# Optimization experiments

Hardware: AMD Instinct MI355X
Metric: run time of the kernel (lower is better)

Reference implementation:

```python
import jax, jax.numpy as jnp
import numpy as np

T, B, N_IN, N_OUT = 100, 32, 1024, 512
LR_LTP, LR_LTD = 1e-4, -1e-4
TAU_PRE, TAU_POST, DT = 20.0, 20.0, 1.0
W_MIN, W_MAX = 0.0, 1.0
SPIKE_PROB = 0.05


def setup_inputs() -> dict:
    key = jax.random.key(0)
    k1, k2, k3 = jax.random.split(key, 3)
    weight = jax.random.uniform(k1, (N_OUT, N_IN), dtype=jnp.float32)
    pre_spikes = (jax.random.uniform(k2, (T, B, N_IN)) < SPIKE_PROB).astype(jnp.float32)
    post_spikes = (jax.random.uniform(k3, (T, B, N_OUT)) < SPIKE_PROB).astype(jnp.float32)
    pre_trace = jnp.zeros((B, N_IN), jnp.float32)
    post_trace = jnp.zeros((B, N_OUT), jnp.float32)
    return {"weight": weight, "pre_spikes": pre_spikes, "post_spikes": post_spikes,
            "pre_trace": pre_trace, "post_trace": post_trace}


def reference(weight, pre_spikes, post_spikes, pre_trace, post_trace):
    # weight: [N_out, N_in]; pre_spikes: [T,B,N_in]; post_spikes: [T,B,N_out]
    decay_pre = jnp.exp(jnp.asarray(-DT / TAU_PRE, weight.dtype))
    decay_post = jnp.exp(jnp.asarray(-DT / TAU_POST, weight.dtype))
    # Soft bounds (w_max=1.0 > 0 -> w_max - w; w_min=0.0 not < 0 -> w)
    soft_ltp = W_MAX - weight
    soft_ltd = weight
    Bf = jnp.asarray(pre_spikes.shape[1], weight.dtype)

    def step(carry, xs):
        pre_tr, post_tr, dw = carry
        pre_s, post_s = xs  # [B,N_in], [B,N_out]
        pre_tr = pre_tr * decay_pre + pre_s
        post_tr = post_tr * decay_post + post_s
        # batch-mean of outer products -> [N_out, N_in]
        ltp_mean = jnp.einsum('bo,bi->oi', post_s, pre_tr) / Bf
        ltd_mean = jnp.einsum('bo,bi->oi', post_tr, pre_s) / Bf
        dw = dw + LR_LTP * soft_ltp * ltp_mean + LR_LTD * soft_ltd * ltd_mean
        return (pre_tr, post_tr, dw), None

    init = (pre_trace, post_trace, jnp.zeros_like(weight))
    (pre_tr, post_tr, delta_w), _ = jax.lax.scan(step, init, (pre_spikes, post_spikes))
    return delta_w, pre_tr, post_tr
```

## Files before the change

### kernel.cpp

```cpp
#include <hip/hip_runtime.h>

typedef unsigned short ushort;
typedef unsigned int uint;
typedef __attribute__((ext_vector_type(8))) short short8;
typedef __attribute__((ext_vector_type(4))) float floatx4;

#define T_STEPS 100
#define BATCH   32
#define NIN     1024
#define NOUT    512

#define SEG     112
#define KPAD    (BATCH * SEG)
#define KROWB   (KPAD * 2)
#define KS      16
#define KCHUNK  (KPAD / KS)
#define BK      32

#define LR_LTP  (1e-4f)
#define LR_LTD  (-1e-4f)
#define INV_B   (1.0f / 32.0f)
#define DECAY   0.951229424500714f
#define D28     0.246596963941607f
#define TCH     28
#define NCHUNK  4

#define OFF_PRE  (NOUT * NIN)
#define OFF_POST (OFF_PRE + BATCH * NIN)

#define U_PRST  0
#define U_PRTT  (U_PRST + NIN * KPAD)
#define U_POST  (U_PRTT + NIN * KPAD)
#define U_POTT  (U_POST + NOUT * KPAD)
#define U_END   (U_POTT + NOUT * KPAD)

static __device__ __forceinline__ ushort f2bf(float f) {
    union { float f; unsigned int u; } v; v.f = f;
    unsigned int r = (v.u + 0x7FFFu + ((v.u >> 16) & 1u)) >> 16;
    return (ushort)r;
}

__global__ __launch_bounds__(256) void stdp_traces_t(
    const float* __restrict__ pre_s,
    const float* __restrict__ post_s,
    const float* __restrict__ pre_tr0,
    const float* __restrict__ post_tr0,
    ushort* __restrict__ pre_s_t, ushort* __restrict__ pre_tr_t,
    ushort* __restrict__ post_s_t, ushort* __restrict__ post_tr_t,
    float* __restrict__ out)
{
    __shared__ float Eend[NCHUNK][64];

    const int chain = threadIdx.x & 63;
    const int c     = threadIdx.x >> 6;
    const int g     = blockIdx.x * 64 + chain;

    const float* src; const float* init;
    ushort *dstS, *dstT;
    int id, nch, shift, outoff;
    if (g < BATCH * NIN) {
        src = pre_s;  init = pre_tr0;  dstS = pre_s_t;  dstT = pre_tr_t;
        id = g;               nch = NIN;  shift = 10; outoff = OFF_PRE;
    } else {
        src = post_s; init = post_tr0; dstS = post_s_t; dstT = post_tr_t;
        id = g - BATCH * NIN; nch = NOUT; shift = 9;  outoff = OFF_POST;
    }

    const int stride = BATCH * nch;
    const int t0 = c * TCH;

    float x[TCH];
    uint  sp[TCH / 2];
    #pragma unroll
    for (int m = 0; m < TCH; m += 2) {
        float v0 = (t0 + m     < T_STEPS) ? src[(size_t)(t0 + m)     * stride + id] : 0.f;
        float v1 = (t0 + m + 1 < T_STEPS) ? src[(size_t)(t0 + m + 1) * stride + id] : 0.f;
        x[m] = v0; x[m + 1] = v1;
        sp[m / 2] = (uint)f2bf(v0) | ((uint)f2bf(v1) << 16);
    }

    float e = 0.f;
    #pragma unroll
    for (int m = 0; m < TCH; ++m) { e = e * DECAY + x[m]; x[m] = e; }
    Eend[c][chain] = e;
    __syncthreads();

    float C = init[id];
    for (int cc = 0; cc < c; ++cc) C = C * D28 + Eend[cc][chain];
    float p = C * DECAY;
    #pragma unroll
    for (int m = 0; m < TCH; ++m) { x[m] += p; p *= DECAY; }

    if (c == NCHUNK - 1) out[outoff + id] = x[15];

    uint tp[TCH / 2];
    #pragma unroll
    for (int m = 0; m < TCH; m += 2)
        tp[m / 2] = (uint)f2bf(x[m]) | ((uint)f2bf(x[m + 1]) << 16);

    const int b  = id >> shift;
    const int ch = id & (nch - 1);
    ushort* ps = dstS + (size_t)ch * KPAD + b * SEG + c * TCH;
    ushort* pt = dstT + (size_t)ch * KPAD + b * SEG + c * TCH;
    #pragma unroll
    for (int j = 0; j < 7; ++j) {
        ((uint2*)ps)[j] = make_uint2(sp[2 * j], sp[2 * j + 1]);
        ((uint2*)pt)[j] = make_uint2(tp[2 * j], tp[2 * j + 1]);
    }
}

__global__ __launch_bounds__(256) void stdp_gemm_dual(
    const ushort* __restrict__ post_s_t, const ushort* __restrict__ pre_tr_t,
    const ushort* __restrict__ post_tr_t, const ushort* __restrict__ pre_s_t,
    const float* __restrict__ wmat, float* __restrict__ Spart)
{
    __shared__ ushort AsP[128 * 32];
    __shared__ ushort AsD[128 * 32];
    __shared__ ushort BsP[128 * 32];
    __shared__ ushort BsD[128 * 32];

    const int i0 = blockIdx.x * 128;
    const int o0 = blockIdx.y * 128;
    const int k0 = blockIdx.z * KCHUNK;

    const int tid  = threadIdx.x;
    const int w    = tid >> 6;
    const int lane = tid & 63;
    const int quad = lane >> 4;
    const int l16  = lane & 15;
    const int wm   = w & 1;
    const int wn   = w >> 1;

    floatx4 accP[4][4], accD[4][4];
    const floatx4 zero4 = {0.f, 0.f, 0.f, 0.f};
    #pragma unroll
    for (int mt = 0; mt < 4; ++mt)
        #pragma unroll
        for (int nt = 0; nt < 4; ++nt) { accP[mt][nt] = zero4; accD[mt][nt] = zero4; }

    for (int kb = k0; kb < k0 + KCHUNK; kb += BK) {
        #pragma unroll
        for (int q = 0; q < 2; ++q) {
            const int c   = w * 128 + q * 64 + lane;
            const int row = c >> 2;
            const int kob = (c & 3) * 16;
            const size_t aoff = (size_t)(o0 + row) * KROWB + kb * 2 + kob;
            const size_t boff = (size_t)(i0 + row) * KROWB + kb * 2 + kob;
            const int ldso = w * 2048 + q * 1024;
            __builtin_amdgcn_global_load_lds(
                (const __attribute__((address_space(1))) void*)((const char*)post_s_t + aoff),
                (__attribute__((address_space(3))) void*)((char*)AsP + ldso), 16, 0, 0);
            __builtin_amdgcn_global_load_lds(
                (const __attribute__((address_space(1))) void*)((const char*)post_tr_t + aoff),
                (__attribute__((address_space(3))) void*)((char*)AsD + ldso), 16, 0, 0);
            __builtin_amdgcn_global_load_lds(
                (const __attribute__((address_space(1))) void*)((const char*)pre_tr_t + boff),
                (__attribute__((address_space(3))) void*)((char*)BsP + ldso), 16, 0, 0);
            __builtin_amdgcn_global_load_lds(
                (const __attribute__((address_space(1))) void*)((const char*)pre_s_t + boff),
                (__attribute__((address_space(3))) void*)((char*)BsD + ldso), 16, 0, 0);
        }
        __syncthreads();

        short8 aP[4], aD[4], bP[4], bD[4];
        #pragma unroll
        for (int mt = 0; mt < 4; ++mt) {
            const int r = (wm * 64 + mt * 16 + l16) * 32 + quad * 8;
            aP[mt] = *(const short8*)&AsP[r];
            aD[mt] = *(const short8*)&AsD[r];
        }
        #pragma unroll
        for (int nt = 0; nt < 4; ++nt) {
            const int r = (wn * 64 + nt * 16 + l16) * 32 + quad * 8;
            bP[nt] = *(const short8*)&BsP[r];
            bD[nt] = *(const short8*)&BsD[r];
        }
        #pragma unroll
        for (int mt = 0; mt < 4; ++mt)
            #pragma unroll
            for (int nt = 0; nt < 4; ++nt) {
                accP[mt][nt] = __builtin_amdgcn_mfma_f32_16x16x32_bf16(
                    aP[mt], bP[nt], accP[mt][nt], 0, 0, 0);
                accD[mt][nt] = __builtin_amdgcn_mfma_f32_16x16x32_bf16(
                    aD[mt], bD[nt], accD[mt][nt], 0, 0, 0);
            }
        __syncthreads();
    }

    float* Sz = Spart + (size_t)blockIdx.z * (NOUT * NIN);
    const float c1 = LR_LTP * INV_B;
    const float c2 = LR_LTD * INV_B;
    #pragma unroll
    for (int mt = 0; mt < 4; ++mt) {
        const int obase = o0 + wm * 64 + mt * 16 + quad * 4;
        #pragma unroll
        for (int nt = 0; nt < 4; ++nt) {
            const int i = i0 + wn * 64 + nt * 16 + l16;
            #pragma unroll
            for (int r = 0; r < 4; ++r) {
                const size_t idx = (size_t)(obase + r) * NIN + i;
                const float wv = wmat[idx];
                Sz[idx] = c1 * (1.0f - wv) * accP[mt][nt][r]
                        + c2 * wv          * accD[mt][nt][r];
            }
        }
    }
}

__global__ __launch_bounds__(256) void stdp_finalize(
    const float* __restrict__ Spart, float* __restrict__ out)
{
    const int j = blockIdx.x * blockDim.x + threadIdx.x;
    float4 s = make_float4(0.f, 0.f, 0.f, 0.f);
    #pragma unroll
    for (int z = 0; z < KS; ++z) {
        const float4 p = ((const float4*)(Spart + (size_t)z * (NOUT * NIN)))[j];
        s.x += p.x; s.y += p.y; s.z += p.z; s.w += p.w;
    }
    ((float4*)out)[j] = s;
}

extern "C" void kernel_launch(void* const* d_in, const int* in_sizes, int n_in,
                              void* d_out, int out_size, void* d_ws, size_t ws_size,
                              hipStream_t stream) {
    const float* weight   = (const float*)d_in[0];
    const float* pre_s    = (const float*)d_in[1];
    const float* post_s   = (const float*)d_in[2];
    const float* pre_tr0  = (const float*)d_in[3];
    const float* post_tr0 = (const float*)d_in[4];
    float* out = (float*)d_out;

    ushort* u = (ushort*)d_ws;
    ushort* pre_s_t   = u + U_PRST;
    ushort* pre_tr_t  = u + U_PRTT;
    ushort* post_s_t  = u + U_POST;
    ushort* post_tr_t = u + U_POTT;
    float*  Spart     = (float*)((char*)d_ws + (size_t)U_END * 2);

    stdp_traces_t<<<dim3(BATCH * (NIN + NOUT) / 64), dim3(256), 0, stream>>>(
        pre_s, post_s, pre_tr0, post_tr0,
        pre_s_t, pre_tr_t, post_s_t, post_tr_t, out);

    stdp_gemm_dual<<<dim3(NIN / 128, NOUT / 128, KS), dim3(256), 0, stream>>>(
        post_s_t, pre_tr_t, post_tr_t, pre_s_t, weight, Spart);

    stdp_finalize<<<dim3((NOUT * NIN / 4) / 256), dim3(256), 0, stream>>>(
        Spart, out);
}
```

Baseline: 119.7 us.

## Stage transposed spike/trace tiles in LDS for coalesced writes and pad strides

The trace kernel now writes its bf16 spike and trace rows into shared memory first, then issues 16-byte coalesced stores to the transposed global buffers instead of scattered 8-byte per-thread stores. The K row stride of the transposed buffers is padded from 3584 to 3648 elements, and the per-split partial-sum slabs are offset by 64 floats, to avoid channel/bank aliasing on power-of-two strides. This adds LDS usage and an extra barrier in the trace kernel. The GEMM loads rely on KROWB, so they now read with the padded stride.

```diff
diff --git a/kernel.cpp b/kernel.cpp
--- a/kernel.cpp
+++ b/kernel.cpp
@@ -12,7 +12,8 @@
 
 #define SEG     112
 #define KPAD    (BATCH * SEG)
-#define KROWB   (KPAD * 2)
+#define KSTRIDE 3648
+#define KROWB   (KSTRIDE * 2)
 #define KS      16
 #define KCHUNK  (KPAD / KS)
 #define BK      32
@@ -24,15 +25,17 @@
 #define D28     0.246596963941607f
 #define TCH     28
 #define NCHUNK  4
+#define LROW    120
 
 #define OFF_PRE  (NOUT * NIN)
 #define OFF_POST (OFF_PRE + BATCH * NIN)
 
 #define U_PRST  0
-#define U_PRTT  (U_PRST + NIN * KPAD)
-#define U_POST  (U_PRTT + NIN * KPAD)
-#define U_POTT  (U_POST + NOUT * KPAD)
-#define U_END   (U_POTT + NOUT * KPAD)
+#define U_PRTT  (U_PRST + NIN * KSTRIDE)
+#define U_POST  (U_PRTT + NIN * KSTRIDE)
+#define U_POTT  (U_POST + NOUT * KSTRIDE)
+#define U_END   (U_POTT + NOUT * KSTRIDE)
+#define SLABF   (NOUT * NIN + 64)
 
 static __device__ __forceinline__ ushort f2bf(float f) {
     union { float f; unsigned int u; } v; v.f = f;
@@ -49,6 +52,8 @@
     ushort* __restrict__ post_s_t, ushort* __restrict__ post_tr_t,
     float* __restrict__ out)
 {
+    __shared__ __align__(16) ushort Ls[64 * LROW];
+    __shared__ __align__(16) ushort Lt[64 * LROW];
     __shared__ float Eend[NCHUNK][64];
 
     const int chain = threadIdx.x & 63;
@@ -56,19 +61,16 @@
     const int g     = blockIdx.x * 64 + chain;
 
     const float* src; const float* init;
-    ushort *dstS, *dstT;
-    int id, nch, shift, outoff;
+    int id, stride, outoff;
     if (g < BATCH * NIN) {
-        src = pre_s;  init = pre_tr0;  dstS = pre_s_t;  dstT = pre_tr_t;
-        id = g;               nch = NIN;  shift = 10; outoff = OFF_PRE;
+        src = pre_s;  init = pre_tr0;
+        id = g;               stride = BATCH * NIN;  outoff = OFF_PRE;
     } else {
-        src = post_s; init = post_tr0; dstS = post_s_t; dstT = post_tr_t;
-        id = g - BATCH * NIN; nch = NOUT; shift = 9;  outoff = OFF_POST;
-    }
-
-    const int stride = BATCH * nch;
+        src = post_s; init = post_tr0;
+        id = g - BATCH * NIN; stride = BATCH * NOUT; outoff = OFF_POST;
+    }
+
     const int t0 = c * TCH;
-
     float x[TCH];
     uint  sp[TCH / 2];
     #pragma unroll
@@ -93,19 +95,39 @@
 
     if (c == NCHUNK - 1) out[outoff + id] = x[15];
 
-    uint tp[TCH / 2];
-    #pragma unroll
-    for (int m = 0; m < TCH; m += 2)
-        tp[m / 2] = (uint)f2bf(x[m]) | ((uint)f2bf(x[m + 1]) << 16);
-
-    const int b  = id >> shift;
-    const int ch = id & (nch - 1);
-    ushort* ps = dstS + (size_t)ch * KPAD + b * SEG + c * TCH;
-    ushort* pt = dstT + (size_t)ch * KPAD + b * SEG + c * TCH;
+    {
+        ushort* ls = Ls + chain * LROW + c * TCH;
+        ushort* lt = Lt + chain * LROW + c * TCH;
+        #pragma unroll
+        for (int j = 0; j < 7; ++j) {
+            const float x0 = x[2 * j * 2];
+            (void)x0;
+            ((uint2*)ls)[j] = make_uint2(sp[2 * j], sp[2 * j + 1]);
+            const uint t_lo = (uint)f2bf(x[4 * j])     | ((uint)f2bf(x[4 * j + 1]) << 16);
+            const uint t_hi = (uint)f2bf(x[4 * j + 2]) | ((uint)f2bf(x[4 * j + 3]) << 16);
+            ((uint2*)lt)[j] = make_uint2(t_lo, t_hi);
+        }
+    }
+    __syncthreads();
+
+    int id0 = blockIdx.x * 64;
+    ushort *dS, *dT; int b0, ch0;
+    if (id0 < BATCH * NIN) {
+        b0 = id0 >> 10; ch0 = id0 & 1023; dS = pre_s_t;  dT = pre_tr_t;
+    } else {
+        const int idq = id0 - BATCH * NIN;
+        b0 = idq >> 9;  ch0 = idq & 511;  dS = post_s_t; dT = post_tr_t;
+    }
     #pragma unroll
     for (int j = 0; j < 7; ++j) {
-        ((uint2*)ps)[j] = make_uint2(sp[2 * j], sp[2 * j + 1]);
-        ((uint2*)pt)[j] = make_uint2(tp[2 * j], tp[2 * j + 1]);
+        const int q  = threadIdx.x + 256 * j;
+        const int op = q >= 896;
+        const int qq = q - op * 896;
+        const int r  = qq / 14;
+        const int cc = qq - r * 14;
+        const ushort* lsrc = (op ? Lt : Ls) + r * LROW + cc * 8;
+        ushort* gdst = (op ? dT : dS) + (size_t)(ch0 + r) * KSTRIDE + b0 * SEG + cc * 8;
+        *(uint4*)gdst = *(const uint4*)lsrc;
     }
 }
 
@@ -187,7 +209,7 @@
         __syncthreads();
     }
 
-    float* Sz = Spart + (size_t)blockIdx.z * (NOUT * NIN);
+    float* Sz = Spart + (size_t)blockIdx.z * SLABF;
     const float c1 = LR_LTP * INV_B;
     const float c2 = LR_LTD * INV_B;
     #pragma unroll
@@ -214,7 +236,7 @@
     float4 s = make_float4(0.f, 0.f, 0.f, 0.f);
     #pragma unroll
     for (int z = 0; z < KS; ++z) {
-        const float4 p = ((const float4*)(Spart + (size_t)z * (NOUT * NIN)))[j];
+        const float4 p = ((const float4*)(Spart + (size_t)z * SLABF))[j];
         s.x += p.x; s.y += p.y; s.z += p.z; s.w += p.w;
     }
     ((float4*)out)[j] = s;
```

New measurement: 114.5 us. 1.05x faster.
